# Kernel optimization log

Measured on AMD Instinct MI355X. Metric: run time of the kernel, lower is better.

Reference implementation:

```python
import jax, jax.numpy as jnp
import numpy as np

IN_FEATURES = 4096
RANK = 64
NUM_EXPERTS = 8
ALPHA = 64.0
SPARSITY = 0.8
SCALING = ALPHA / RANK  # alpha / rank


def setup_inputs() -> dict:
    key = jax.random.key(0)
    k1, k2, k3, k4 = jax.random.split(key, 4)
    B, S = 4, 4096
    projected_input = jax.random.normal(k1, (B, S, RANK), dtype=jnp.float32)
    routing_weights = jax.random.uniform(k2, (B, S, NUM_EXPERTS), dtype=jnp.float32)
    # Stacked expert A matrices [K, in_features, rank] (kaiming-like init ~ normal here)
    A = jax.random.normal(k3, (NUM_EXPERTS, IN_FEATURES, RANK), dtype=jnp.float32) * 0.02
    sparse_mask = (jax.random.uniform(k4, (NUM_EXPERTS, IN_FEATURES, RANK)) >= SPARSITY).astype(jnp.float32)
    A = A * sparse_mask  # module masks A at init as well
    return {
        "projected_input": projected_input,
        "routing_weights": routing_weights,
        "A": A,
        "sparse_mask": sparse_mask,
    }


def reference(projected_input, routing_weights, A, sparse_mask):
    # A_sparse[k] = A[k] * mask[k]; per expert: scaling * (p @ A_sparse[k].T)
    # then weighted sum over experts with routing_weights[..., k].
    A_eff = (A * sparse_mask) * SCALING          # [k, d, r]
    # Weight the rank-projected input per expert, then contract:
    # wp[b,s,k,r] = routing_weights[b,s,k] * projected_input[b,s,r]
    wp = jnp.einsum("bsk,bsr->bskr", routing_weights, projected_input)
    out = jnp.einsum("bskr,kdr->bsd", wp, A_eff)  # [b, s, in_features]
    return out
```

## Files before the change

### kernel.cpp

```cpp
#include <hip/hip_runtime.h>

#define IN_FEATURES 4096
#define RANK 64
#define NUM_EXPERTS 8
#define KDIM 512
#define TOKENS 16384
#define SCALING 1.0f

#define BM 256
#define BN 128
#define BK 32
#define NKT (KDIM / BK)

typedef __bf16 bf16x8 __attribute__((ext_vector_type(8)));
typedef float f32x4 __attribute__((ext_vector_type(4)));

__device__ __forceinline__ unsigned short f2bf(float f) {
  union { float f; unsigned int u; } v; v.f = f;
  unsigned int u = v.u;
  u += 0x7fffu + ((u >> 16) & 1u);
  return (unsigned short)(u >> 16);
}

__device__ __forceinline__ void gload_lds16(const unsigned short* g, unsigned short* l) {
  __builtin_amdgcn_global_load_lds(
      (const __attribute__((address_space(1))) void*)g,
      (__attribute__((address_space(3))) void*)l,
      16, 0, 0);
}

#define QN4 ((long)TOKENS * KDIM / 4)
#define BN4 ((long)IN_FEATURES * KDIM / 4)
__global__ void __launch_bounds__(256) pack_both(
    const float* __restrict__ p, const float* __restrict__ w,
    const float* __restrict__ A, const float* __restrict__ mask,
    unsigned short* __restrict__ q, unsigned short* __restrict__ Bt) {
  long gid = (long)blockIdx.x * 256 + threadIdx.x;
  if (gid < QN4) {
    int idx = (int)gid;
    int t = idx >> 7;
    int k = (idx >> 4) & 7;
    int r0 = (idx & 15) * 4;
    float wk = w[t * NUM_EXPERTS + k];
    float4 pv = *(const float4*)&p[t * RANK + r0];
    ushort4 o;
    o.x = f2bf(wk * pv.x);
    o.y = f2bf(wk * pv.y);
    o.z = f2bf(wk * pv.z);
    o.w = f2bf(wk * pv.w);
    *(ushort4*)&q[(long)t * KDIM + k * RANK + r0] = o;
  } else {
    int idx = (int)(gid - QN4);
    int d = idx >> 7;
    int k = (idx >> 4) & 7;
    int r0 = (idx & 15) * 4;
    long src = ((long)k * IN_FEATURES + d) * RANK + r0;
    float4 a = *(const float4*)&A[src];
    float4 m = *(const float4*)&mask[src];
    ushort4 o;
    o.x = f2bf(a.x * m.x * SCALING);
    o.y = f2bf(a.y * m.y * SCALING);
    o.z = f2bf(a.z * m.z * SCALING);
    o.w = f2bf(a.w * m.w * SCALING);
    *(ushort4*)&Bt[(long)d * KDIM + k * RANK + r0] = o;
  }
}

__global__ void __launch_bounds__(512, 4) gemm_kernel(
    const unsigned short* __restrict__ q,
    const unsigned short* __restrict__ Bt,
    float* __restrict__ out) {
  __shared__ __align__(16) unsigned short sA[2][BM * BK];
  __shared__ __align__(16) unsigned short sB[2][BN * BK];

  const int tid = threadIdx.x;
  const int lane = tid & 63;
  const int wid = tid >> 6;
  const int u = lane & 15;
  const int quad = lane >> 4;
  const int wave_m = (wid >> 2) * 128;
  const int wave_n = (wid & 3) * 32;

  const int m0 = blockIdx.x * BM;
  const int n0 = blockIdx.y * BN;

  f32x4 acc[8][2];
#pragma unroll
  for (int i = 0; i < 8; ++i)
#pragma unroll
    for (int j = 0; j < 2; ++j)
      acc[i][j] = (f32x4){0.f, 0.f, 0.f, 0.f};

  const int cA0 = tid, cA1 = tid + 512, cB = tid;
  const int rA0 = cA0 >> 2, rA1 = cA1 >> 2, rBr = cB >> 2;
  const int lgA0 = (cA0 & 3) ^ ((rA0 >> 1) & 3);
  const int lgA1 = (cA1 & 3) ^ ((rA1 >> 1) & 3);
  const int lgB  = (cB  & 3) ^ ((rBr >> 1) & 3);
  const unsigned short* gA0 = q  + (m0 + rA0) * KDIM + lgA0 * 8;
  const unsigned short* gA1 = q  + (m0 + rA1) * KDIM + lgA1 * 8;
  const unsigned short* gB  = Bt + (n0 + rBr) * KDIM + lgB  * 8;
  const int lA0 = cA0 * 8, lA1 = cA1 * 8, lB = cB * 8;

  auto stage = [&](int buf, int kt) {
    int ko = (kt & (NKT - 1)) * BK;
    gload_lds16(gA0 + ko, &sA[buf][lA0]);
    gload_lds16(gA1 + ko, &sA[buf][lA1]);
    gload_lds16(gB + ko, &sB[buf][lB]);
  };

  stage(0, 0);
  __syncthreads();

  const int physv = quad ^ ((u >> 1) & 3);

  for (int kt = 0; kt < NKT; ++kt) {
    const int buf = kt & 1;
    stage(buf ^ 1, kt + 1);

    const unsigned short* bA = sA[buf];
    const unsigned short* bB = sB[buf];

    bf16x8 bfr[2];
#pragma unroll
    for (int g = 0; g < 2; ++g) {
      int r = wave_n + g * 16 + u;
      bfr[g] = *(const bf16x8*)&bB[r * BK + physv * 8];
    }
#pragma unroll
    for (int h = 0; h < 2; ++h) {
      bf16x8 af[4];
#pragma unroll
      for (int f = 0; f < 4; ++f) {
        int r = wave_m + (h * 4 + f) * 16 + u;
        af[f] = *(const bf16x8*)&bA[r * BK + physv * 8];
      }
#pragma unroll
      for (int f = 0; f < 4; ++f)
#pragma unroll
        for (int g = 0; g < 2; ++g)
          acc[h * 4 + f][g] = __builtin_amdgcn_mfma_f32_16x16x32_bf16(
              af[f], bfr[g], acc[h * 4 + f][g], 0, 0, 0);
    }
    __syncthreads();
  }

#pragma unroll
  for (int f = 0; f < 8; ++f) {
    int row = m0 + wave_m + f * 16 + quad * 4;
#pragma unroll
    for (int rr = 0; rr < 4; ++rr) {
      float* orow = out + (long)(row + rr) * IN_FEATURES + n0 + wave_n + u;
#pragma unroll
      for (int g = 0; g < 2; ++g)
        orow[g * 16] = acc[f][g][rr];
    }
  }
}

extern "C" void kernel_launch(void* const* d_in, const int* in_sizes, int n_in,
                              void* d_out, int out_size, void* d_ws, size_t ws_size,
                              hipStream_t stream) {
  const float* p    = (const float*)d_in[0];
  const float* w    = (const float*)d_in[1];
  const float* A    = (const float*)d_in[2];
  const float* mask = (const float*)d_in[3];
  float* out = (float*)d_out;

  unsigned short* q  = (unsigned short*)d_ws;
  unsigned short* Bt = q + (size_t)TOKENS * KDIM;

  int pack_blocks = (int)((QN4 + BN4) / 256);
  pack_both<<<pack_blocks, 256, 0, stream>>>(p, w, A, mask, q, Bt);

  dim3 grid(TOKENS / BM, IN_FEATURES / BN);
  gemm_kernel<<<grid, dim3(512), 0, stream>>>(q, Bt, out);
}
```

Baseline: 342.6 us.

## Fuse routing-weighted input packing into GEMM A-tile load

The separate pre-pass that wrote the routing-weighted bf16 activation matrix q (16384x512) is removed. The GEMM now loads fp32 projected_input and routing weights directly, multiplies and converts to bf16 in registers, and writes the A tile to LDS after the MFMAs, prefetching one step ahead. This avoids writing and re-reading a 16 MB intermediate, at the cost of extra register pressure, VALU conversion work in the GEMM main loop, and replacing async global-to-LDS loads for A with register round-trips.

```diff
diff --git a/kernel.cpp b/kernel.cpp
--- a/kernel.cpp
+++ b/kernel.cpp
@@ -29,45 +29,28 @@
       16, 0, 0);
 }
 
-#define QN4 ((long)TOKENS * KDIM / 4)
 #define BN4 ((long)IN_FEATURES * KDIM / 4)
-__global__ void __launch_bounds__(256) pack_both(
-    const float* __restrict__ p, const float* __restrict__ w,
+__global__ void __launch_bounds__(256) b_pack(
     const float* __restrict__ A, const float* __restrict__ mask,
-    unsigned short* __restrict__ q, unsigned short* __restrict__ Bt) {
-  long gid = (long)blockIdx.x * 256 + threadIdx.x;
-  if (gid < QN4) {
-    int idx = (int)gid;
-    int t = idx >> 7;
-    int k = (idx >> 4) & 7;
-    int r0 = (idx & 15) * 4;
-    float wk = w[t * NUM_EXPERTS + k];
-    float4 pv = *(const float4*)&p[t * RANK + r0];
-    ushort4 o;
-    o.x = f2bf(wk * pv.x);
-    o.y = f2bf(wk * pv.y);
-    o.z = f2bf(wk * pv.z);
-    o.w = f2bf(wk * pv.w);
-    *(ushort4*)&q[(long)t * KDIM + k * RANK + r0] = o;
-  } else {
-    int idx = (int)(gid - QN4);
-    int d = idx >> 7;
-    int k = (idx >> 4) & 7;
-    int r0 = (idx & 15) * 4;
-    long src = ((long)k * IN_FEATURES + d) * RANK + r0;
-    float4 a = *(const float4*)&A[src];
-    float4 m = *(const float4*)&mask[src];
-    ushort4 o;
-    o.x = f2bf(a.x * m.x * SCALING);
-    o.y = f2bf(a.y * m.y * SCALING);
-    o.z = f2bf(a.z * m.z * SCALING);
-    o.w = f2bf(a.w * m.w * SCALING);
-    *(ushort4*)&Bt[(long)d * KDIM + k * RANK + r0] = o;
-  }
+    unsigned short* __restrict__ Bt) {
+  int idx = blockIdx.x * 256 + threadIdx.x;
+  int d = idx >> 7;
+  int k = (idx >> 4) & 7;
+  int r0 = (idx & 15) * 4;
+  long src = ((long)k * IN_FEATURES + d) * RANK + r0;
+  float4 a = *(const float4*)&A[src];
+  float4 m = *(const float4*)&mask[src];
+  ushort4 o;
+  o.x = f2bf(a.x * m.x * SCALING);
+  o.y = f2bf(a.y * m.y * SCALING);
+  o.z = f2bf(a.z * m.z * SCALING);
+  o.w = f2bf(a.w * m.w * SCALING);
+  *(ushort4*)&Bt[(long)d * KDIM + k * RANK + r0] = o;
 }
 
 __global__ void __launch_bounds__(512, 4) gemm_kernel(
-    const unsigned short* __restrict__ q,
+    const float* __restrict__ p,
+    const float* __restrict__ w,
     const unsigned short* __restrict__ Bt,
     float* __restrict__ out) {
   __shared__ __align__(16) unsigned short sA[2][BM * BK];
@@ -96,26 +79,55 @@
   const int lgA0 = (cA0 & 3) ^ ((rA0 >> 1) & 3);
   const int lgA1 = (cA1 & 3) ^ ((rA1 >> 1) & 3);
   const int lgB  = (cB  & 3) ^ ((rBr >> 1) & 3);
-  const unsigned short* gA0 = q  + (m0 + rA0) * KDIM + lgA0 * 8;
-  const unsigned short* gA1 = q  + (m0 + rA1) * KDIM + lgA1 * 8;
-  const unsigned short* gB  = Bt + (n0 + rBr) * KDIM + lgB  * 8;
+  const float* pR0 = p + (m0 + rA0) * RANK + lgA0 * 8;
+  const float* pR1 = p + (m0 + rA1) * RANK + lgA1 * 8;
+  const float* wR0 = w + (m0 + rA0) * NUM_EXPERTS;
+  const float* wR1 = w + (m0 + rA1) * NUM_EXPERTS;
+  const unsigned short* gB = Bt + (n0 + rBr) * KDIM + lgB * 8;
   const int lA0 = cA0 * 8, lA1 = cA1 * 8, lB = cB * 8;
 
-  auto stage = [&](int buf, int kt) {
-    int ko = (kt & (NKT - 1)) * BK;
-    gload_lds16(gA0 + ko, &sA[buf][lA0]);
-    gload_lds16(gA1 + ko, &sA[buf][lA1]);
-    gload_lds16(gB + ko, &sB[buf][lB]);
+  auto stageB = [&](int buf, int kt) {
+    gload_lds16(gB + (kt & (NKT - 1)) * BK, &sB[buf][lB]);
   };
-
-  stage(0, 0);
-  __syncthreads();
+  auto loadA = [&](int kt, f32x4 (&pv)[2][2], float (&wv)[2]) {
+    int kw = kt & (NKT - 1);
+    int rb = (kw & 1) * BK;
+    int e  = kw >> 1;
+    pv[0][0] = *(const f32x4*)(pR0 + rb);
+    pv[0][1] = *(const f32x4*)(pR0 + rb + 4);
+    pv[1][0] = *(const f32x4*)(pR1 + rb);
+    pv[1][1] = *(const f32x4*)(pR1 + rb + 4);
+    wv[0] = wR0[e];
+    wv[1] = wR1[e];
+  };
+  auto writeA = [&](int buf, f32x4 (&pv)[2][2], float (&wv)[2]) {
+    unsigned short tmp[2][8];
+#pragma unroll
+    for (int h = 0; h < 2; ++h)
+#pragma unroll
+      for (int j = 0; j < 2; ++j)
+#pragma unroll
+        for (int x = 0; x < 4; ++x)
+          tmp[h][j * 4 + x] = f2bf(wv[h] * pv[h][j][x]);
+    *(bf16x8*)&sA[buf][lA0] = *(bf16x8*)tmp[0];
+    *(bf16x8*)&sA[buf][lA1] = *(bf16x8*)tmp[1];
+  };
 
   const int physv = quad ^ ((u >> 1) & 3);
 
+  {
+    f32x4 pv[2][2]; float wv[2];
+    stageB(0, 0);
+    loadA(0, pv, wv);
+    writeA(0, pv, wv);
+  }
+  __syncthreads();
+
   for (int kt = 0; kt < NKT; ++kt) {
     const int buf = kt & 1;
-    stage(buf ^ 1, kt + 1);
+    stageB(buf ^ 1, kt + 1);
+    f32x4 pv[2][2]; float wv[2];
+    loadA(kt + 1, pv, wv);
 
     const unsigned short* bA = sA[buf];
     const unsigned short* bB = sB[buf];
@@ -141,6 +153,8 @@
           acc[h * 4 + f][g] = __builtin_amdgcn_mfma_f32_16x16x32_bf16(
               af[f], bfr[g], acc[h * 4 + f][g], 0, 0, 0);
     }
+
+    writeA(buf ^ 1, pv, wv);
     __syncthreads();
   }
 
@@ -166,12 +180,10 @@
   const float* mask = (const float*)d_in[3];
   float* out = (float*)d_out;
 
-  unsigned short* q  = (unsigned short*)d_ws;
-  unsigned short* Bt = q + (size_t)TOKENS * KDIM;
+  unsigned short* Bt = (unsigned short*)d_ws;
 
-  int pack_blocks = (int)((QN4 + BN4) / 256);
-  pack_both<<<pack_blocks, 256, 0, stream>>>(p, w, A, mask, q, Bt);
+  b_pack<<<(int)(BN4 / 256), 256, 0, stream>>>(A, mask, Bt);
 
   dim3 grid(TOKENS / BM, IN_FEATURES / BN);
-  gemm_kernel<<<grid, dim3(512), 0, stream>>>(q, Bt, out);
+  gemm_kernel<<<grid, dim3(512), 0, stream>>>(p, w, Bt, out);
 }
```

New measurement: 353.7 us. 3.2% more time.
